# Kernel tuning notes

Measured on AMD Instinct MI355X. Metric: run time of the kernel, lower is better.

Reference implementation:

```python
import jax, jax.numpy as jnp
import numpy as np

DIM = 192
HRES, WRES = 64, 64
NUM_HEADS = 6
WS = 8  # window_size
MLP_HIDDEN = int(DIM * 4.0)
EPS = 1e-5


def layer_norm(x, gamma, beta):
    mu = jnp.mean(x, axis=-1, keepdims=True)
    var = jnp.var(x, axis=-1, keepdims=True)
    return (x - mu) * jax.lax.rsqrt(var + EPS) * gamma + beta


def window_partition(x, ws):
    B, H, W, C = x.shape
    x = x.reshape(B, H // ws, ws, W // ws, ws, C)
    x = jnp.transpose(x, (0, 1, 3, 2, 4, 5))
    return x.reshape(-1, ws * ws, C)


def window_reverse(windows, ws, H, W, C):
    B = windows.shape[0] // ((H // ws) * (W // ws))
    x = windows.reshape(B, H // ws, W // ws, ws, ws, C)
    x = jnp.transpose(x, (0, 1, 3, 2, 4, 5))
    return x.reshape(B, H, W, C)


def setup_inputs() -> dict:
    key = jax.random.key(0)
    ks = jax.random.split(key, 12)
    s = 0.02
    return {
        "x": jax.random.normal(ks[0], (32, HRES * WRES, DIM), dtype=jnp.float32),
        "norm1_g": jnp.ones((DIM,), jnp.float32),
        "norm1_b": jnp.zeros((DIM,), jnp.float32),
        "qkv_w": jax.random.normal(ks[1], (DIM, 3 * DIM), jnp.float32) * s,
        "qkv_b": jnp.zeros((3 * DIM,), jnp.float32),
        "proj_w": jax.random.normal(ks[2], (DIM, DIM), jnp.float32) * s,
        "proj_b": jnp.zeros((DIM,), jnp.float32),
        "norm2_g": jnp.ones((DIM,), jnp.float32),
        "norm2_b": jnp.zeros((DIM,), jnp.float32),
        "fc1_w": jax.random.normal(ks[3], (DIM, MLP_HIDDEN), jnp.float32) * s,
        "fc1_b": jnp.zeros((MLP_HIDDEN,), jnp.float32),
        "fc2_w": jax.random.normal(ks[4], (MLP_HIDDEN, DIM), jnp.float32) * s,
        "fc2_b": jnp.zeros((DIM,), jnp.float32),
    }


def reference(x, norm1_g, norm1_b, qkv_w, qkv_b, proj_w, proj_b,
              norm2_g, norm2_b, fc1_w, fc1_b, fc2_w, fc2_b):
    B, L, C = x.shape
    H, W = HRES, WRES
    hd = C // NUM_HEADS
    scale = hd ** -0.5

    shortcut = x
    h = layer_norm(x, norm1_g, norm1_b).reshape(B, H, W, C)
    win = window_partition(h, WS)  # [nW*B, WS*WS, C]
    Bw, N, _ = win.shape

    qkv = (win @ qkv_w + qkv_b).reshape(Bw, N, 3, NUM_HEADS, hd)
    q, k, v = jnp.transpose(qkv, (2, 0, 3, 1, 4))  # each [Bw, H, N, hd]
    attn = jnp.einsum('bhnd,bhmd->bhnm', q, k) * scale
    attn = jax.nn.softmax(attn, axis=-1)
    out = jnp.einsum('bhnm,bhmd->bhnd', attn, v)
    out = jnp.transpose(out, (0, 2, 1, 3)).reshape(Bw, N, C)
    out = out @ proj_w + proj_b

    h = window_reverse(out, WS, H, W, C).reshape(B, L, C)
    x = shortcut + h

    m = layer_norm(x, norm2_g, norm2_b)
    m = jax.nn.gelu(m @ fc1_w + fc1_b, approximate=False)
    m = m @ fc2_w + fc2_b
    return x + m
```

## Files before the change

### kernel.cpp

```cpp
#include <hip/hip_runtime.h>
#include <hip/hip_bf16.h>
#include <math.h>

#define DIM   192
#define NH    6
#define HD    32
#define WSZ   8
#define HRES_ 64
#define WRES_ 64
#define BATCH 32
#define LTOK  (HRES_*WRES_)
#define MTOK  (BATCH*LTOK)
#define QKVN  (3*DIM)
#define MLPH  (4*DIM)

using bf16 = __hip_bfloat16;
using bf16x8 = __attribute__((ext_vector_type(8))) short;
using f32x4  = __attribute__((ext_vector_type(4))) float;

__device__ __forceinline__ float bf2f(bf16 h) { return __bfloat162float(h); }
__device__ __forceinline__ float us2f(unsigned short u) {
    union { unsigned u32; float f; } c; c.u32 = ((unsigned)u) << 16; return c.f;
}

__global__ void detect_kernel(const unsigned short* __restrict__ g, int* __restrict__ flag)
{
    *flag = (g[0] == 0x3F80) ? 0 : 1;
}

__global__ __launch_bounds__(256) void cvt_kernel(
    const void* __restrict__ src, bf16* __restrict__ dst,
    long n, long elem_off, const int* __restrict__ flag)
{
    long i = ((long)blockIdx.x * 256 + threadIdx.x) * 8;
    if (i >= n) return;
    if (i + 8 <= n) {
        if (*flag) {
            const float* s = (const float*)src + elem_off + i;
            float4 a = *reinterpret_cast<const float4*>(s);
            float4 b = *reinterpret_cast<const float4*>(s + 4);
            bf16 o[8];
            o[0]=__float2bfloat16(a.x); o[1]=__float2bfloat16(a.y);
            o[2]=__float2bfloat16(a.z); o[3]=__float2bfloat16(a.w);
            o[4]=__float2bfloat16(b.x); o[5]=__float2bfloat16(b.y);
            o[6]=__float2bfloat16(b.z); o[7]=__float2bfloat16(b.w);
            *reinterpret_cast<bf16x8*>(dst + i) = *reinterpret_cast<const bf16x8*>(o);
        } else {
            *reinterpret_cast<bf16x8*>(dst + i) =
                *reinterpret_cast<const bf16x8*>((const bf16*)src + elem_off + i);
        }
    } else {
        for (long k2 = i; k2 < n; ++k2) {
            if (*flag) dst[k2] = __float2bfloat16(((const float*)src)[elem_off + k2]);
            else       dst[k2] = ((const bf16*)src)[elem_off + k2];
        }
    }
}

__global__ __launch_bounds__(256) void store_kernel(
    const bf16* __restrict__ src, void* __restrict__ dst,
    long n, long elem_off, const int* __restrict__ flag)
{
    long i = ((long)blockIdx.x * 256 + threadIdx.x) * 8;
    if (i >= n) return;
    if (i + 8 <= n) {
        bf16x8 v = *reinterpret_cast<const bf16x8*>(src + i);
        if (*flag) {
            float* d = (float*)dst + elem_off + i;
            float4 a, b;
            a.x = us2f((unsigned short)v[0]); a.y = us2f((unsigned short)v[1]);
            a.z = us2f((unsigned short)v[2]); a.w = us2f((unsigned short)v[3]);
            b.x = us2f((unsigned short)v[4]); b.y = us2f((unsigned short)v[5]);
            b.z = us2f((unsigned short)v[6]); b.w = us2f((unsigned short)v[7]);
            *reinterpret_cast<float4*>(d)     = a;
            *reinterpret_cast<float4*>(d + 4) = b;
        } else {
            *reinterpret_cast<bf16x8*>((bf16*)dst + elem_off + i) = v;
        }
    } else {
        for (long k2 = i; k2 < n; ++k2) {
            if (*flag) ((float*)dst)[elem_off + k2] = bf2f(src[k2]);
            else       ((bf16*)dst)[elem_off + k2] = src[k2];
        }
    }
}

__global__ __launch_bounds__(256) void ln_kernel(
    const bf16* __restrict__ x, const bf16* __restrict__ g,
    const bf16* __restrict__ b, bf16* __restrict__ y)
{
    int wave = threadIdx.x >> 6;
    int lane = threadIdx.x & 63;
    long token = (long)blockIdx.x * 4 + wave;
    const bf16* xp = x + token * DIM;
    float f0 = bf2f(xp[lane]);
    float f1 = bf2f(xp[lane + 64]);
    float f2 = bf2f(xp[lane + 128]);
    float s  = f0 + f1 + f2;
    float ss = f0*f0 + f1*f1 + f2*f2;
    #pragma unroll
    for (int m = 1; m < 64; m <<= 1) { s += __shfl_xor(s, m); ss += __shfl_xor(ss, m); }
    float mean = s * (1.0f/192.0f);
    float var  = ss * (1.0f/192.0f) - mean*mean;
    float rstd = rsqrtf(var + 1e-5f);
    bf16* yp = y + token * DIM;
    yp[lane]       = __float2bfloat16((f0-mean)*rstd*bf2f(g[lane])       + bf2f(b[lane]));
    yp[lane + 64]  = __float2bfloat16((f1-mean)*rstd*bf2f(g[lane + 64])  + bf2f(b[lane + 64]));
    yp[lane + 128] = __float2bfloat16((f2-mean)*rstd*bf2f(g[lane + 128]) + bf2f(b[lane + 128]));
}

__global__ void transpose_kernel(const bf16* __restrict__ in, bf16* __restrict__ out,
                                 int K, int N)
{
    int idx = blockIdx.x * 256 + threadIdx.x;
    if (idx < K * N) {
        int n = idx % N, k = idx / N;
        out[n * K + k] = in[idx];
    }
}

template<int EPI>
__global__ __launch_bounds__(256) void gemm_bt(
    const bf16* __restrict__ A, const bf16* __restrict__ Bt,
    const bf16* __restrict__ bias, const bf16* __restrict__ res,
    bf16* __restrict__ C, int M, int N, int K)
{
    constexpr int KC = 192;
    __shared__ __align__(16) bf16 bsh[(KC/32) * 4 * 64 * 8];
    int tid  = threadIdx.x;
    int wave = tid >> 6, lane = tid & 63;
    int t = lane & 15, q = lane >> 4;
    int  n0 = blockIdx.x * 64;
    long m0 = (long)blockIdx.y * 128;

    f32x4 acc[2][4] = {};

    for (int kc = 0; kc < K; kc += KC) {
        __syncthreads();
        for (int s = tid; s < (KC/32) * 256; s += 256) {
            int ks  = s >> 8;
            int rem = s & 255;
            int j   = rem >> 6;
            int ln  = rem & 63;
            int tt = ln & 15, qq = ln >> 4;
            int n = j * 16 + tt;
            int k = ks * 32 + qq * 8;
            const float4* src = reinterpret_cast<const float4*>(
                Bt + (long)(n0 + n) * K + kc + k);
            reinterpret_cast<float4*>(bsh)[s] = *src;
        }
        __syncthreads();

        const bf16* arow = A + (m0 + wave * 32 + t) * (long)K + kc + q * 8;
        #pragma unroll
        for (int ks = 0; ks < KC/32; ++ks) {
            bf16x8 a0 = *reinterpret_cast<const bf16x8*>(arow + ks * 32);
            bf16x8 a1 = *reinterpret_cast<const bf16x8*>(arow + 16 * (long)K + ks * 32);
            #pragma unroll
            for (int j = 0; j < 4; ++j) {
                bf16x8 b = reinterpret_cast<const bf16x8*>(bsh)[ks * 256 + j * 64 + lane];
                acc[0][j] = __builtin_amdgcn_mfma_f32_16x16x32_bf16(a0, b, acc[0][j], 0, 0, 0);
                acc[1][j] = __builtin_amdgcn_mfma_f32_16x16x32_bf16(a1, b, acc[1][j], 0, 0, 0);
            }
        }
    }

    #pragma unroll
    for (int j = 0; j < 4; ++j) {
        int col = n0 + j * 16 + t;
        float bv = bf2f(bias[col]);
        #pragma unroll
        for (int i = 0; i < 2; ++i) {
            #pragma unroll
            for (int r = 0; r < 4; ++r) {
                long row = m0 + wave * 32 + i * 16 + q * 4 + r;
                float v = acc[i][j][r] + bv;
                if (EPI == 1) v = v * 0.5f * (1.0f + erff(v * 0.70710678118f));
                if (EPI == 2) v += bf2f(res[row * N + col]);
                C[row * N + col] = __float2bfloat16(v);
            }
        }
    }
}

__global__ __launch_bounds__(256) void mlp_kernel(
    const bf16* __restrict__ A,   const bf16* __restrict__ W1t,
    const bf16* __restrict__ b1,  const bf16* __restrict__ W2t,
    const bf16* __restrict__ b2,  const bf16* __restrict__ res,
    bf16* __restrict__ out, int M)
{
    __shared__ __align__(16) bf16 bsh[6 * 4 * 64 * 8];
    __shared__ __align__(16) bf16 hsh[128 * 200];
    int tid  = threadIdx.x;
    int wave = tid >> 6, lane = tid & 63;
    int t = lane & 15, q = lane >> 4;
    long m0 = (long)blockIdx.x * 128;

    bf16x8 a_reg[2][6];
    #pragma unroll
    for (int i = 0; i < 2; ++i) {
        const bf16* ap = A + (m0 + wave * 32 + i * 16 + t) * (long)DIM + q * 8;
        #pragma unroll
        for (int ks = 0; ks < 6; ++ks)
            a_reg[i][ks] = *reinterpret_cast<const bf16x8*>(ap + ks * 32);
    }

    f32x4 oacc[2][12] = {};

    for (int nc = 0; nc < 4; ++nc) {
        for (int j64 = 0; j64 < 3; ++j64) {
            __syncthreads();
            #pragma unroll
            for (int it = 0; it < 6; ++it) {
                int s   = it * 256 + tid;
                int ks  = s >> 8;
                int rem = s & 255;
                int j   = rem >> 6;
                int ln  = rem & 63;
                int n   = nc * 192 + j64 * 64 + j * 16 + (ln & 15);
                int k   = ks * 32 + (ln >> 4) * 8;
                reinterpret_cast<float4*>(bsh)[s] =
                    *reinterpret_cast<const float4*>(W1t + (long)n * DIM + k);
            }
            __syncthreads();

            f32x4 hacc[2][4] = {};
            #pragma unroll
            for (int ks = 0; ks < 6; ++ks) {
                #pragma unroll
                for (int j = 0; j < 4; ++j) {
                    bf16x8 b = reinterpret_cast<const bf16x8*>(bsh)[ks * 256 + j * 64 + lane];
                    hacc[0][j] = __builtin_amdgcn_mfma_f32_16x16x32_bf16(a_reg[0][ks], b, hacc[0][j], 0, 0, 0);
                    hacc[1][j] = __builtin_amdgcn_mfma_f32_16x16x32_bf16(a_reg[1][ks], b, hacc[1][j], 0, 0, 0);
                }
            }
            #pragma unroll
            for (int j = 0; j < 4; ++j) {
                int cl = j64 * 64 + j * 16 + t;
                float bv = bf2f(b1[nc * 192 + cl]);
                #pragma unroll
                for (int i = 0; i < 2; ++i) {
                    #pragma unroll
                    for (int r = 0; r < 4; ++r) {
                        int row = wave * 32 + i * 16 + q * 4 + r;
                        float v = hacc[i][j][r] + bv;
                        v = v * 0.5f * (1.0f + erff(v * 0.70710678118f));
                        hsh[row * 200 + cl] = __float2bfloat16(v);
                    }
                }
            }
        }

        for (int j64 = 0; j64 < 3; ++j64) {
            __syncthreads();
            #pragma unroll
            for (int it = 0; it < 6; ++it) {
                int s   = it * 256 + tid;
                int ks  = s >> 8;
                int rem = s & 255;
                int j   = rem >> 6;
                int ln  = rem & 63;
                int n   = j64 * 64 + j * 16 + (ln & 15);
                int k   = nc * 192 + ks * 32 + (ln >> 4) * 8;
                reinterpret_cast<float4*>(bsh)[s] =
                    *reinterpret_cast<const float4*>(W2t + (long)n * MLPH + k);
            }
            __syncthreads();

            #pragma unroll
            for (int ks = 0; ks < 6; ++ks) {
                bf16x8 h0 = *reinterpret_cast<const bf16x8*>(hsh + (wave * 32 + t) * 200 + ks * 32 + q * 8);
                bf16x8 h1 = *reinterpret_cast<const bf16x8*>(hsh + (wave * 32 + 16 + t) * 200 + ks * 32 + q * 8);
                #pragma unroll
                for (int j = 0; j < 4; ++j) {
                    bf16x8 b = reinterpret_cast<const bf16x8*>(bsh)[ks * 256 + j * 64 + lane];
                    oacc[0][j64 * 4 + j] = __builtin_amdgcn_mfma_f32_16x16x32_bf16(h0, b, oacc[0][j64 * 4 + j], 0, 0, 0);
                    oacc[1][j64 * 4 + j] = __builtin_amdgcn_mfma_f32_16x16x32_bf16(h1, b, oacc[1][j64 * 4 + j], 0, 0, 0);
                }
            }
        }
    }

    #pragma unroll
    for (int jj = 0; jj < 12; ++jj) {
        int col = (jj >> 2) * 64 + (jj & 3) * 16 + t;
        float bv = bf2f(b2[col]);
        #pragma unroll
        for (int i = 0; i < 2; ++i) {
            #pragma unroll
            for (int r = 0; r < 4; ++r) {
                long row = m0 + wave * 32 + i * 16 + q * 4 + r;
                float v = oacc[i][jj][r] + bv + bf2f(res[row * DIM + col]);
                out[row * DIM + col] = __float2bfloat16(v);
            }
        }
    }
}

__global__ __launch_bounds__(256) void attn_kernel(
    const bf16* __restrict__ qkv, bf16* __restrict__ out)
{
    int win  = blockIdx.x;
    int head = blockIdx.y;
    __shared__ __align__(16) bf16 qs[64 * 32];
    __shared__ __align__(16) bf16 ksm[64 * 32];
    __shared__ __align__(16) bf16 vt[32 * 64];
    __shared__ __align__(16) bf16 ps[64 * 64];
    __shared__ int nat[64];

    int tid  = threadIdx.x;
    int wave = tid >> 6, lane = tid & 63;
    int t = lane & 15, q = lane >> 4;

    if (tid < 64) {
        int b = win >> 6;
        int widx = win & 63;
        int wh = widx >> 3, ww = widx & 7;
        int r = wh * 8 + (tid >> 3);
        int c = ww * 8 + (tid & 7);
        nat[tid] = b * LTOK + r * WRES_ + c;
    }
    __syncthreads();

    {
        int token = tid >> 2, ch = tid & 3;
        long base = (long)nat[token] * QKVN + head * HD + ch * 8;
        float4 qv = *reinterpret_cast<const float4*>(qkv + base);
        float4 kv = *reinterpret_cast<const float4*>(qkv + base + DIM);
        float4 vv = *reinterpret_cast<const float4*>(qkv + base + 2 * DIM);
        *reinterpret_cast<float4*>(qs  + token * 32 + ch * 8) = qv;
        *reinterpret_cast<float4*>(ksm + token * 32 + ch * 8) = kv;
        const bf16* vp = reinterpret_cast<const bf16*>(&vv);
        #pragma unroll
        for (int e = 0; e < 8; ++e) vt[(ch * 8 + e) * 64 + token] = vp[e];
    }
    __syncthreads();

    f32x4 sacc[4] = {};
    {
        bf16x8 aq = *reinterpret_cast<const bf16x8*>(qs + (wave * 16 + t) * 32 + q * 8);
        #pragma unroll
        for (int j = 0; j < 4; ++j) {
            bf16x8 bk = *reinterpret_cast<const bf16x8*>(ksm + (j * 16 + t) * 32 + q * 8);
            sacc[j] = __builtin_amdgcn_mfma_f32_16x16x32_bf16(aq, bk, sacc[j], 0, 0, 0);
        }
    }

    const float scale = 0.17677669529663689f;
    #pragma unroll
    for (int r = 0; r < 4; ++r) {
        float m_ = fmaxf(fmaxf(sacc[0][r], sacc[1][r]), fmaxf(sacc[2][r], sacc[3][r]));
        #pragma unroll
        for (int msk = 1; msk < 16; msk <<= 1) m_ = fmaxf(m_, __shfl_xor(m_, msk));
        float p[4], sum = 0.f;
        #pragma unroll
        for (int j = 0; j < 4; ++j) { p[j] = expf((sacc[j][r] - m_) * scale); sum += p[j]; }
        #pragma unroll
        for (int msk = 1; msk < 16; msk <<= 1) sum += __shfl_xor(sum, msk);
        float inv = 1.0f / sum;
        int row = wave * 16 + q * 4 + r;
        #pragma unroll
        for (int j = 0; j < 4; ++j)
            ps[row * 64 + j * 16 + t] = __float2bfloat16(p[j] * inv);
    }
    __syncthreads();

    f32x4 oacc[2] = {};
    #pragma unroll
    for (int kk = 0; kk < 2; ++kk) {
        bf16x8 ap = *reinterpret_cast<const bf16x8*>(ps + (wave * 16 + t) * 64 + kk * 32 + q * 8);
        #pragma unroll
        for (int j = 0; j < 2; ++j) {
            bf16x8 bv = *reinterpret_cast<const bf16x8*>(vt + (j * 16 + t) * 64 + kk * 32 + q * 8);
            oacc[j] = __builtin_amdgcn_mfma_f32_16x16x32_bf16(ap, bv, oacc[j], 0, 0, 0);
        }
    }
    #pragma unroll
    for (int j = 0; j < 2; ++j) {
        #pragma unroll
        for (int r = 0; r < 4; ++r) {
            int row = wave * 16 + q * 4 + r;
            out[(long)nat[row] * DIM + head * HD + j * 16 + t] = __float2bfloat16(oacc[j][r]);
        }
    }
}

extern "C" void kernel_launch(void* const* d_in, const int* in_sizes, int n_in,
                              void* d_out, int out_size, void* d_ws, size_t ws_size,
                              hipStream_t stream)
{
    char* ws = (char*)d_ws;
    size_t off = 0;
    auto alloc = [&](size_t bytes) {
        char* p = ws + off;
        off += (bytes + 255) & ~(size_t)255;
        return p;
    };

    int* flag = (int*)alloc(sizeof(int));

    static const int psz[12] = { DIM, DIM, DIM*QKVN, QKVN, DIM*DIM, DIM,
                                 DIM, DIM, DIM*MLPH, MLPH, MLPH*DIM, DIM };
    bf16* par[12];
    for (int i = 0; i < 12; ++i) par[i] = (bf16*)alloc((size_t)psz[i] * 2);
    bf16 *n1g = par[0], *n1b = par[1], *qkvw = par[2], *qkvb = par[3],
         *projw = par[4], *projb = par[5], *n2g = par[6], *n2b = par[7],
         *fc1w = par[8], *fc1b = par[9], *fc2w = par[10], *fc2b = par[11];

    bf16* wqkv_t  = (bf16*)alloc((size_t)QKVN * DIM * 2);
    bf16* wproj_t = (bf16*)alloc((size_t)DIM * DIM * 2);
    bf16* wfc1_t  = (bf16*)alloc((size_t)MLPH * DIM * 2);
    bf16* wfc2_t  = (bf16*)alloc((size_t)DIM * MLPH * 2);
    size_t fixed_off = off;

    int C = 32;
    while (C > 1) {
        size_t Mc = (size_t)C * LTOK;
        if (fixed_off + Mc * 2304 + 4096 <= ws_size) break;
        C >>= 1;
    }
    size_t Mc = (size_t)C * LTOK;
    bf16* xb = (bf16*)alloc(Mc * 384);
    bf16* R  = (bf16*)alloc(Mc * 384);
    bf16* Y  = (bf16*)alloc(Mc * 384);
    bf16* S  = (bf16*)alloc(Mc * 1152);
    int nchunks = BATCH / C;

    detect_kernel<<<1, 1, 0, stream>>>((const unsigned short*)d_in[1], flag);

    for (int i = 0; i < 12; ++i) {
        unsigned blocks = (unsigned)(((long)psz[i] + 8*256 - 1) / (8*256));
        cvt_kernel<<<blocks, 256, 0, stream>>>(d_in[i + 1], par[i], psz[i], 0, flag);
    }

    transpose_kernel<<<(DIM*QKVN + 255)/256, 256, 0, stream>>>(qkvw, wqkv_t, DIM, QKVN);
    transpose_kernel<<<(DIM*DIM  + 255)/256, 256, 0, stream>>>(projw, wproj_t, DIM, DIM);
    transpose_kernel<<<(DIM*MLPH + 255)/256, 256, 0, stream>>>(fc1w, wfc1_t, DIM, MLPH);
    transpose_kernel<<<(MLPH*DIM + 255)/256, 256, 0, stream>>>(fc2w, wfc2_t, MLPH, DIM);

    for (int ci = 0; ci < nchunks; ++ci) {
        long eoff = (long)ci * Mc * DIM;
        long nelem = (long)Mc * DIM;
        unsigned vblocks = (unsigned)((nelem + 8*256 - 1) / (8*256));

        cvt_kernel<<<vblocks, 256, 0, stream>>>(d_in[0], xb, nelem, eoff, flag);
        ln_kernel<<<(unsigned)(Mc/4), 256, 0, stream>>>(xb, n1g, n1b, R);
        gemm_bt<0><<<dim3(QKVN/64, Mc/128), 256, 0, stream>>>(R, wqkv_t, qkvb, nullptr, S, (int)Mc, QKVN, DIM);
        attn_kernel<<<dim3(C*64, NH), 256, 0, stream>>>(S, R);
        gemm_bt<2><<<dim3(DIM/64, Mc/128), 256, 0, stream>>>(R, wproj_t, projb, xb, Y, (int)Mc, DIM, DIM);
        ln_kernel<<<(unsigned)(Mc/4), 256, 0, stream>>>(Y, n2g, n2b, R);
        mlp_kernel<<<(unsigned)(Mc/128), 256, 0, stream>>>(R, wfc1_t, fc1b, wfc2_t, fc2b, Y, Y, (int)Mc);
        store_kernel<<<vblocks, 256, 0, stream>>>(Y, d_out, nelem, eoff, flag);
    }
}
```

Before: 810.1 us.

## Restructure fused MLP into 64-wide hidden chunks with smaller hidden LDS buffer

```diff
diff --git a/kernel.cpp b/kernel.cpp
--- a/kernel.cpp
+++ b/kernel.cpp
@@ -189,8 +189,9 @@
     const bf16* __restrict__ b2,  const bf16* __restrict__ res,
     bf16* __restrict__ out, int M)
 {
-    __shared__ __align__(16) bf16 bsh[6 * 4 * 64 * 8];
-    __shared__ __align__(16) bf16 hsh[128 * 200];
+    constexpr int HS = 88;
+    __shared__ __align__(16) bf16 bsh[1536 * 8];
+    __shared__ __align__(16) bf16 hsh[128 * HS];
     int tid  = threadIdx.x;
     int wave = tid >> 6, lane = tid & 63;
     int t = lane & 15, q = lane >> 4;
@@ -207,90 +208,85 @@
 
     f32x4 oacc[2][12] = {};
 
-    for (int nc = 0; nc < 4; ++nc) {
-        for (int j64 = 0; j64 < 3; ++j64) {
-            __syncthreads();
-            #pragma unroll
-            for (int it = 0; it < 6; ++it) {
-                int s   = it * 256 + tid;
-                int ks  = s >> 8;
-                int rem = s & 255;
-                int j   = rem >> 6;
-                int ln  = rem & 63;
-                int n   = nc * 192 + j64 * 64 + j * 16 + (ln & 15);
-                int k   = ks * 32 + (ln >> 4) * 8;
-                reinterpret_cast<float4*>(bsh)[s] =
-                    *reinterpret_cast<const float4*>(W1t + (long)n * DIM + k);
-            }
-            __syncthreads();
-
-            f32x4 hacc[2][4] = {};
-            #pragma unroll
-            for (int ks = 0; ks < 6; ++ks) {
+    for (int nc = 0; nc < 12; ++nc) {
+        __syncthreads();
+        #pragma unroll
+        for (int it = 0; it < 6; ++it) {
+            int s   = it * 256 + tid;
+            int ks  = s >> 8;
+            int rem = s & 255;
+            int j   = rem >> 6;
+            int ln  = rem & 63;
+            int n   = nc * 64 + j * 16 + (ln & 15);
+            int k   = ks * 32 + (ln >> 4) * 8;
+            reinterpret_cast<float4*>(bsh)[s] =
+                *reinterpret_cast<const float4*>(W1t + (long)n * DIM + k);
+        }
+        __syncthreads();
+
+        f32x4 hacc[2][4] = {};
+        #pragma unroll
+        for (int ks = 0; ks < 6; ++ks) {
+            #pragma unroll
+            for (int j = 0; j < 4; ++j) {
+                bf16x8 b = reinterpret_cast<const bf16x8*>(bsh)[ks * 256 + j * 64 + lane];
+                hacc[0][j] = __builtin_amdgcn_mfma_f32_16x16x32_bf16(a_reg[0][ks], b, hacc[0][j], 0, 0, 0);
+                hacc[1][j] = __builtin_amdgcn_mfma_f32_16x16x32_bf16(a_reg[1][ks], b, hacc[1][j], 0, 0, 0);
+            }
+        }
+        #pragma unroll
+        for (int j = 0; j < 4; ++j) {
+            float bv = bf2f(b1[nc * 64 + j * 16 + t]);
+            #pragma unroll
+            for (int i = 0; i < 2; ++i) {
                 #pragma unroll
-                for (int j = 0; j < 4; ++j) {
-                    bf16x8 b = reinterpret_cast<const bf16x8*>(bsh)[ks * 256 + j * 64 + lane];
-                    hacc[0][j] = __builtin_amdgcn_mfma_f32_16x16x32_bf16(a_reg[0][ks], b, hacc[0][j], 0, 0, 0);
-                    hacc[1][j] = __builtin_amdgcn_mfma_f32_16x16x32_bf16(a_reg[1][ks], b, hacc[1][j], 0, 0, 0);
+                for (int r = 0; r < 4; ++r) {
+                    int row = wave * 32 + i * 16 + q * 4 + r;
+                    float v = hacc[i][j][r] + bv;
+                    v = v * 0.5f * (1.0f + erff(v * 0.70710678118f));
+                    hsh[row * HS + j * 16 + t] = __float2bfloat16(v);
                 }
             }
-            #pragma unroll
-            for (int j = 0; j < 4; ++j) {
-                int cl = j64 * 64 + j * 16 + t;
-                float bv = bf2f(b1[nc * 192 + cl]);
-                #pragma unroll
-                for (int i = 0; i < 2; ++i) {
-                    #pragma unroll
-                    for (int r = 0; r < 4; ++r) {
-                        int row = wave * 32 + i * 16 + q * 4 + r;
-                        float v = hacc[i][j][r] + bv;
-                        v = v * 0.5f * (1.0f + erff(v * 0.70710678118f));
-                        hsh[row * 200 + cl] = __float2bfloat16(v);
-                    }
-                }
-            }
-        }
-
-        for (int j64 = 0; j64 < 3; ++j64) {
-            __syncthreads();
-            #pragma unroll
-            for (int it = 0; it < 6; ++it) {
-                int s   = it * 256 + tid;
-                int ks  = s >> 8;
-                int rem = s & 255;
-                int j   = rem >> 6;
-                int ln  = rem & 63;
-                int n   = j64 * 64 + j * 16 + (ln & 15);
-                int k   = nc * 192 + ks * 32 + (ln >> 4) * 8;
-                reinterpret_cast<float4*>(bsh)[s] =
-                    *reinterpret_cast<const float4*>(W2t + (long)n * MLPH + k);
-            }
-            __syncthreads();
-
-            #pragma unroll
-            for (int ks = 0; ks < 6; ++ks) {
-                bf16x8 h0 = *reinterpret_cast<const bf16x8*>(hsh + (wave * 32 + t) * 200 + ks * 32 + q * 8);
-                bf16x8 h1 = *reinterpret_cast<const bf16x8*>(hsh + (wave * 32 + 16 + t) * 200 + ks * 32 + q * 8);
-                #pragma unroll
-                for (int j = 0; j < 4; ++j) {
-                    bf16x8 b = reinterpret_cast<const bf16x8*>(bsh)[ks * 256 + j * 64 + lane];
-                    oacc[0][j64 * 4 + j] = __builtin_amdgcn_mfma_f32_16x16x32_bf16(h0, b, oacc[0][j64 * 4 + j], 0, 0, 0);
-                    oacc[1][j64 * 4 + j] = __builtin_amdgcn_mfma_f32_16x16x32_bf16(h1, b, oacc[1][j64 * 4 + j], 0, 0, 0);
-                }
-            }
-        }
-    }
-
-    #pragma unroll
-    for (int jj = 0; jj < 12; ++jj) {
-        int col = (jj >> 2) * 64 + (jj & 3) * 16 + t;
+        }
+        __syncthreads();
+
+        #pragma unroll
+        for (int it = 0; it < 6; ++it) {
+            int s   = it * 256 + tid;
+            int ks  = s / 768;
+            int rem = s - ks * 768;
+            int j   = rem >> 6;
+            int ln  = rem & 63;
+            int n   = j * 16 + (ln & 15);
+            int k   = nc * 64 + ks * 32 + (ln >> 4) * 8;
+            reinterpret_cast<float4*>(bsh)[s] =
+                *reinterpret_cast<const float4*>(W2t + (long)n * MLPH + k);
+        }
+        __syncthreads();
+
+        #pragma unroll
+        for (int ks = 0; ks < 2; ++ks) {
+            bf16x8 h0 = *reinterpret_cast<const bf16x8*>(hsh + (wave * 32 + t) * HS + ks * 32 + q * 8);
+            bf16x8 h1 = *reinterpret_cast<const bf16x8*>(hsh + (wave * 32 + 16 + t) * HS + ks * 32 + q * 8);
+            #pragma unroll
+            for (int j = 0; j < 12; ++j) {
+                bf16x8 b = reinterpret_cast<const bf16x8*>(bsh)[ks * 768 + j * 64 + lane];
+                oacc[0][j] = __builtin_amdgcn_mfma_f32_16x16x32_bf16(h0, b, oacc[0][j], 0, 0, 0);
+                oacc[1][j] = __builtin_amdgcn_mfma_f32_16x16x32_bf16(h1, b, oacc[1][j], 0, 0, 0);
+            }
+        }
+    }
+
+    #pragma unroll
+    for (int j = 0; j < 12; ++j) {
+        int col = j * 16 + t;
         float bv = bf2f(b2[col]);
         #pragma unroll
         for (int i = 0; i < 2; ++i) {
             #pragma unroll
             for (int r = 0; r < 4; ++r) {
                 long row = m0 + wave * 32 + i * 16 + q * 4 + r;
-                float v = oacc[i][jj][r] + bv + bf2f(res[row * DIM + col]);
+                float v = oacc[i][j][r] + bv + bf2f(res[row * DIM + col]);
                 out[row * DIM + col] = __float2bfloat16(v);
             }
         }
```

Result: faster. 791.9 us (-2.2%).
